# Kernel optimization log

Measured on AMD Instinct MI355X. Metric: run time of the kernel, lower is better.

Reference implementation:

```python
import jax, jax.numpy as jnp
import numpy as np
import math

D = 1024
H = 16
HD = D // H


def setup_inputs() -> dict:
    key = jax.random.key(0)
    ks = jax.random.split(key, 12)
    B, L = 2, 2048
    s = 1.0 / math.sqrt(D)
    inp = {
        "q": jax.random.normal(ks[0], (B, L, D), jnp.float32),
        "k": jax.random.normal(ks[1], (B, L, D), jnp.float32),
        "v": jax.random.normal(ks[2], (B, L, D), jnp.float32),
        "Wq": jax.random.normal(ks[3], (D, D), jnp.float32) * s,
        "bq": jnp.zeros((D,), jnp.float32),
        "Wk": jax.random.normal(ks[4], (D, D), jnp.float32) * s,
        "bk": jnp.zeros((D,), jnp.float32),
        "Wv": jax.random.normal(ks[5], (D, D), jnp.float32) * s,
        "bv": jnp.zeros((D,), jnp.float32),
        "Wo": jax.random.normal(ks[6], (D, D), jnp.float32) * s,
        "bo": jnp.zeros((D,), jnp.float32),
        "P": jax.random.normal(ks[7], (H, H), jnp.float32),  # logit_proj_pre
    }
    return inp


def _split_heads(x, B, L):
    # [B,L,D] -> [B,H,L,HD]
    return x.reshape(B, L, H, HD).transpose(0, 2, 1, 3)


def reference(q, k, v, Wq, bq, Wk, bk, Wv, bv, Wo, bo, P):
    B, L, _ = q.shape
    qh = _split_heads(q @ Wq.T + bq, B, L)
    kh = _split_heads(k @ Wk.T + bk, B, L)
    vh = _split_heads(v @ Wv.T + bv, B, L)
    # raw per-head logits [B,H,L,L]
    logits = jnp.einsum("bhld,bhmd->bhlm", qh, kh) / math.sqrt(HD)
    # talking-heads mixing across heads (pre-softmax)
    logits = jnp.einsum("bhlm,hg->bglm", logits, P)
    attn = jax.nn.softmax(logits, axis=-1)
    out = jnp.einsum("bhlm,bhmd->bhld", attn, vh)  # [B,H,L,HD]
    out = out.transpose(0, 2, 1, 3).reshape(B, L, D)
    return out @ Wo.T + bo
```

## Files before the change

kernel.cpp:

```cpp
#include <hip/hip_runtime.h>

#define D_  1024
#define H_  16
#define HD_ 64
#define L_  2048
#define B_  2
#define M_  (B_*L_)

typedef float f32x4  __attribute__((ext_vector_type(4)));
typedef short bf16x4 __attribute__((ext_vector_type(4)));
typedef short bf16x8 __attribute__((ext_vector_type(8)));

#define SRAW_PITCH 20
#define SRAW_SLAB  (16 * SRAW_PITCH)
#define VS_PITCH   24

__device__ __forceinline__ float bf2f(short s) {
    return __uint_as_float(((unsigned int)(unsigned short)s) << 16);
}
__device__ __forceinline__ short f2bf(float f) {
    unsigned u = __float_as_uint(f);
    unsigned r = (u + 0x7FFFu + ((u >> 16) & 1u)) >> 16;
    return (short)r;
}
__device__ __forceinline__ void block_sync() {
    asm volatile("s_waitcnt lgkmcnt(0)" ::: "memory");
    __builtin_amdgcn_sched_barrier(0);
    __builtin_amdgcn_s_barrier();
    __builtin_amdgcn_sched_barrier(0);
}

__global__ __launch_bounds__(256) void proj_mfma(
    const float* __restrict__ q, const float* __restrict__ k, const float* __restrict__ v,
    const float* __restrict__ Wq, const float* __restrict__ bq,
    const float* __restrict__ Wk, const float* __restrict__ bk,
    const float* __restrict__ Wv, const float* __restrict__ bv,
    short* __restrict__ qh, short* __restrict__ qlo,
    short* __restrict__ kh, short* __restrict__ vht)
{
    const int z = blockIdx.z;
    const float* X    = (z == 0) ? q  : (z == 1) ? k  : v;
    const float* W    = (z == 0) ? Wq : (z == 1) ? Wk : Wv;
    const float* bias = (z == 0) ? bq : (z == 1) ? bk : bv;

    __shared__ short Ws[128][72];
    __shared__ short Xs[128][72];

    const int tid  = threadIdx.x;
    const int w    = tid >> 6, lane = tid & 63;
    const int l16  = lane & 15, qq = lane >> 4;
    const int m0   = blockIdx.x * 128;
    const int n0   = blockIdx.y * 128;
    const int ar0  = 64 * (w & 1);
    const int br0  = 64 * (w >> 1);

    f32x4 acc[4][4] = {};

    for (int k0 = 0; k0 < D_; k0 += 64) {
        #pragma unroll
        for (int i = 0; i < 8; ++i) {
            int fidx = i * 256 + tid;
            int r = fidx >> 4, c = fidx & 15;
            float4 wv4 = *(const float4*)(W + (size_t)(n0 + r) * D_ + k0 + c * 4);
            float4 xv4 = *(const float4*)(X + (size_t)(m0 + r) * D_ + k0 + c * 4);
            bf16x4 wb = { f2bf(wv4.x), f2bf(wv4.y), f2bf(wv4.z), f2bf(wv4.w) };
            bf16x4 xb = { f2bf(xv4.x), f2bf(xv4.y), f2bf(xv4.z), f2bf(xv4.w) };
            *(bf16x4*)&Ws[r][c * 4] = wb;
            *(bf16x4*)&Xs[r][c * 4] = xb;
        }
        __syncthreads();
        bf16x8 af[2][4], bfv[2][4];
        #pragma unroll
        for (int kc = 0; kc < 2; ++kc)
            #pragma unroll
            for (int i = 0; i < 4; ++i) {
                const short* Ab = (z < 2) ? &Ws[ar0 + 16 * i + l16][kc * 32 + qq * 8]
                                          : &Xs[ar0 + 16 * i + l16][kc * 32 + qq * 8];
                const short* Bb = (z < 2) ? &Xs[br0 + 16 * i + l16][kc * 32 + qq * 8]
                                          : &Ws[br0 + 16 * i + l16][kc * 32 + qq * 8];
                af[kc][i]  = *(const bf16x8*)Ab;
                bfv[kc][i] = *(const bf16x8*)Bb;
            }
        #pragma unroll
        for (int kc = 0; kc < 2; ++kc)
            #pragma unroll
            for (int i = 0; i < 4; ++i)
                #pragma unroll
                for (int j = 0; j < 4; ++j)
                    acc[i][j] = __builtin_amdgcn_mfma_f32_16x16x32_bf16(af[kc][i], bfv[kc][j], acc[i][j], 0, 0, 0);
        __syncthreads();
    }

    if (z < 2) {
        #pragma unroll
        for (int i = 0; i < 4; ++i) {
            int nb = n0 + ar0 + 16 * i + qq * 4;
            float4 b4 = *(const float4*)(bias + nb);
            int h = nb >> 6, hd = nb & 63;
            #pragma unroll
            for (int j = 0; j < 4; ++j) {
                int m = m0 + br0 + 16 * j + l16;
                int bb = m >> 11, l = m & (L_ - 1);
                size_t o = ((((size_t)bb * H_ + h) * L_) + l) * HD_ + hd;
                f32x4 c = acc[i][j];
                float v0 = c[0] + b4.x, v1 = c[1] + b4.y, v2 = c[2] + b4.z, v3 = c[3] + b4.w;
                bf16x4 hi = { f2bf(v0), f2bf(v1), f2bf(v2), f2bf(v3) };
                if (z == 0) {
                    *(bf16x4*)&qh[o] = hi;
                    bf16x4 lo = { f2bf(v0 - bf2f(hi[0])), f2bf(v1 - bf2f(hi[1])),
                                  f2bf(v2 - bf2f(hi[2])), f2bf(v3 - bf2f(hi[3])) };
                    *(bf16x4*)&qlo[o] = lo;
                } else {
                    *(bf16x4*)&kh[o] = hi;
                }
            }
        }
    } else {
        #pragma unroll
        for (int i = 0; i < 4; ++i) {
            int mb = m0 + ar0 + 16 * i + qq * 4;
            int bb = mb >> 11, lb = mb & (L_ - 1);
            #pragma unroll
            for (int j = 0; j < 4; ++j) {
                int n = n0 + br0 + 16 * j + l16;
                int h = n >> 6, hd = n & 63;
                float bn = bias[n];
                size_t o = (((size_t)bb * H_ + h) * HD_ + hd) * (size_t)L_ + lb;
                f32x4 c = acc[i][j];
                bf16x4 ov = { f2bf(c[0] + bn), f2bf(c[1] + bn), f2bf(c[2] + bn), f2bf(c[3] + bn) };
                *(bf16x4*)&vht[o] = ov;
            }
        }
    }
}

__global__ __launch_bounds__(512, 2) void attn_mfma(
    const short* __restrict__ qh, const short* __restrict__ qlo,
    const short* __restrict__ kh, const short* __restrict__ vht,
    const float* __restrict__ P, short* __restrict__ attn_out,
    float* __restrict__ pacc, float* __restrict__ pms, int ntiles)
{
    __shared__ __align__(16) float Sraw[16 * SRAW_SLAB];
    __shared__ __align__(16) char  UPool[8 * 2 * 64 * VS_PITCH * 2];
    __shared__ float PmS[256];

    float* Smix  = (float*)UPool;
    const int tid  = threadIdx.x;
    const int n    = blockIdx.x;
    const int half = n >> 8;
    const int inr  = n & 255;
    const int b    = (inr >> 2) & 1;
    const int l0   = ((inr >> 3) * 4 + (inr & 3)) * 16;
    const int tb   = half * ntiles;
    const int w    = tid >> 6, lane = tid & 63;
    const int l16  = lane & 15, qq = lane >> 4;
    const size_t hb = (size_t)b * H_;
    short* VslabW = (short*)UPool + w * (2 * 64 * VS_PITCH);

    bf16x8 qf[2][2][2];
    #pragma unroll
    for (int hh = 0; hh < 2; ++hh)
        #pragma unroll
        for (int kc = 0; kc < 2; ++kc) {
            size_t off = ((hb + 2 * w + hh) * L_ + l0 + l16) * HD_ + kc * 32 + qq * 8;
            qf[hh][kc][0] = *(const bf16x8*)(qh  + off);
            qf[hh][kc][1] = *(const bf16x8*)(qlo + off);
        }

    int vgi_[4], vd_[4];
    const int vc = lane & 1;
    #pragma unroll
    for (int i = 0; i < 4; ++i) {
        int vrow = i * 32 + (lane >> 1);
        vgi_[i] = vrow >> 6;
        vd_[i]  = vrow & 63;
    }
    int vwoff[4];
    #pragma unroll
    for (int i = 0; i < 4; ++i)
        vwoff[i] = vgi_[i] * (64 * VS_PITCH) + vd_[i] * VS_PITCH + vc * 8;

    auto kload = [&](int tile, bf16x8 (&kdst)[2][2]) {
        const int mn = (tile & 127) * 16;
        #pragma unroll
        for (int hh = 0; hh < 2; ++hh)
            #pragma unroll
            for (int kc = 0; kc < 2; ++kc)
                kdst[hh][kc] = *(const bf16x8*)(kh + ((hb + 2 * w + hh) * L_ + mn + l16) * HD_ + kc * 32 + qq * 8);
    };
    auto vload = [&](int tile, bf16x8 (&vdst)[4]) {
        const int mn = (tile & 127) * 16;
        #pragma unroll
        for (int i = 0; i < 4; ++i)
            vdst[i] = *(const bf16x8*)(vht + ((hb + 2 * w + vgi_[i]) * HD_ + vd_[i]) * (size_t)L_ + mn + vc * 8);
    };

    bf16x8 kP[2][2], vst[4];
    kload(tb, kP); vload(tb, vst);

    if (tid < 256) PmS[tid] = P[tid] * 0.125f;

    f32x4 acc[2][4];
    #pragma unroll
    for (int dt = 0; dt < 4; ++dt) { acc[0][dt] = (f32x4){0.f,0.f,0.f,0.f}; acc[1][dt] = (f32x4){0.f,0.f,0.f,0.f}; }
    float mrun0 = 0.f, mrun1 = 0.f, srun0 = 0.f, srun1 = 0.f;

    auto qkt = [&](bf16x8 (&kr)[2][2], float* sb) {
        #pragma unroll
        for (int hh = 0; hh < 2; ++hh) {
            f32x4 s = (f32x4){0.f,0.f,0.f,0.f};
            s = __builtin_amdgcn_mfma_f32_16x16x32_bf16(kr[hh][0], qf[hh][0][0], s, 0, 0, 0);
            s = __builtin_amdgcn_mfma_f32_16x16x32_bf16(kr[hh][0], qf[hh][0][1], s, 0, 0, 0);
            s = __builtin_amdgcn_mfma_f32_16x16x32_bf16(kr[hh][1], qf[hh][1][0], s, 0, 0, 0);
            s = __builtin_amdgcn_mfma_f32_16x16x32_bf16(kr[hh][1], qf[hh][1][1], s, 0, 0, 0);
            *(f32x4*)(sb + ((2 * w + hh) * 16 + l16) * SRAW_PITCH + qq * 4) = s;
        }
    };

    qkt(kP, Sraw);
    block_sync();
    kload(tb + 1, kP);

    bf16x4 PAhi, PAlo;
    {
        float p0 = PmS[(qq * 4 + 0) * 16 + l16];
        float p1 = PmS[(qq * 4 + 1) * 16 + l16];
        float p2 = PmS[(qq * 4 + 2) * 16 + l16];
        float p3 = PmS[(qq * 4 + 3) * 16 + l16];
        PAhi = (bf16x4){ f2bf(p0), f2bf(p1), f2bf(p2), f2bf(p3) };
        PAlo = (bf16x4){ f2bf(p0 - bf2f(PAhi[0])), f2bf(p1 - bf2f(PAhi[1])),
                         f2bf(p2 - bf2f(PAhi[2])), f2bf(p3 - bf2f(PAhi[3])) };
    }

    for (int t = 0; t < ntiles; ++t) {
        {
            float2 g0 = *(const float2*)&Sraw[((qq * 4 + 0) * 16 + l16) * SRAW_PITCH + 2 * w];
            float2 g1 = *(const float2*)&Sraw[((qq * 4 + 1) * 16 + l16) * SRAW_PITCH + 2 * w];
            float2 g2 = *(const float2*)&Sraw[((qq * 4 + 2) * 16 + l16) * SRAW_PITCH + 2 * w];
            float2 g3 = *(const float2*)&Sraw[((qq * 4 + 3) * 16 + l16) * SRAW_PITCH + 2 * w];
            #pragma unroll
            for (int mi = 0; mi < 2; ++mi) {
                const int m = 2 * w + mi;
                float sv0 = mi ? g0.y : g0.x;
                float sv1 = mi ? g1.y : g1.x;
                float sv2 = mi ? g2.y : g2.x;
                float sv3 = mi ? g3.y : g3.x;
                bf16x4 bhi = { f2bf(sv0), f2bf(sv1), f2bf(sv2), f2bf(sv3) };
                bf16x4 blo = { f2bf(sv0 - bf2f(bhi[0])), f2bf(sv1 - bf2f(bhi[1])),
                               f2bf(sv2 - bf2f(bhi[2])), f2bf(sv3 - bf2f(bhi[3])) };
                f32x4 c = (f32x4){0.f, 0.f, 0.f, 0.f};
                c = __builtin_amdgcn_mfma_f32_16x16x16bf16_1k(PAhi, bhi, c, 0, 0, 0);
                c = __builtin_amdgcn_mfma_f32_16x16x16bf16_1k(PAhi, blo, c, 0, 0, 0);
                c = __builtin_amdgcn_mfma_f32_16x16x16bf16_1k(PAlo, bhi, c, 0, 0, 0);
                *(f32x4*)(Smix + (m * 16 + l16) * SRAW_PITCH + qq * 4) = c;
            }
        }
        block_sync();
        qkt(kP, Sraw);
        kload(tb + t + 2, kP);
        float sx0[4], sx1[4];
        #pragma unroll
        for (int j = 0; j < 4; ++j) {
            float2 gg = *(const float2*)&Smix[((qq * 4 + j) * 16 + l16) * SRAW_PITCH + 2 * w];
            sx0[j] = gg.x;
            sx1[j] = gg.y;
        }
        float e00 = __expf(sx0[0] - mrun0), e01 = __expf(sx0[1] - mrun0);
        float e02 = __expf(sx0[2] - mrun0), e03 = __expf(sx0[3] - mrun0);
        float e10 = __expf(sx1[0] - mrun1), e11 = __expf(sx1[1] - mrun1);
        float e12 = __expf(sx1[2] - mrun1), e13 = __expf(sx1[3] - mrun1);
        bf16x4 pf0 = { f2bf(e00), f2bf(e01), f2bf(e02), f2bf(e03) };
        bf16x4 pf1 = { f2bf(e10), f2bf(e11), f2bf(e12), f2bf(e13) };
        float t0r = fmaxf(fmaxf(sx0[0], sx0[1]), fmaxf(sx0[2], sx0[3]));
        float t1r = fmaxf(fmaxf(sx1[0], sx1[1]), fmaxf(sx1[2], sx1[3]));
        t0r = fmaxf(t0r, __shfl_xor(t0r, 16)); t0r = fmaxf(t0r, __shfl_xor(t0r, 32));
        t1r = fmaxf(t1r, __shfl_xor(t1r, 16)); t1r = fmaxf(t1r, __shfl_xor(t1r, 32));
        float ps0 = e00 + e01 + e02 + e03, ps1 = e10 + e11 + e12 + e13;
        ps0 += __shfl_xor(ps0, 16); ps0 += __shfl_xor(ps0, 32);
        ps1 += __shfl_xor(ps1, 16); ps1 += __shfl_xor(ps1, 32);
        block_sync();
        #pragma unroll
        for (int i = 0; i < 4; ++i)
            *(bf16x8*)&VslabW[vwoff[i]] = vst[i];
        #pragma unroll
        for (int i = 0; i < 2; ++i) {
            bf16x4 pf = i ? pf1 : pf0;
            #pragma unroll
            for (int dt = 0; dt < 4; ++dt) {
                bf16x4 afr = *(const bf16x4*)&VslabW[i * (64 * VS_PITCH) + (dt * 16 + l16) * VS_PITCH + qq * 4];
                acc[i][dt] = __builtin_amdgcn_mfma_f32_16x16x16bf16_1k(afr, pf, acc[i][dt], 0, 0, 0);
            }
        }
        vload(tb + t + 1, vst);
        float mnew0 = fmaxf(mrun0, t0r), mnew1 = fmaxf(mrun1, t1r);
        float corr0 = __expf(mrun0 - mnew0), corr1 = __expf(mrun1 - mnew1);
        srun0 = (srun0 + ps0) * corr0; srun1 = (srun1 + ps1) * corr1;
        acc[0][0] *= corr0; acc[0][1] *= corr0; acc[0][2] *= corr0; acc[0][3] *= corr0;
        acc[1][0] *= corr1; acc[1][1] *= corr1; acc[1][2] *= corr1; acc[1][3] *= corr1;
        mrun0 = mnew0; mrun1 = mnew1;
        block_sync();
    }

    if (pacc) {
        #pragma unroll
        for (int i = 0; i < 2; ++i) {
            int g = 2 * w + i;
            #pragma unroll
            for (int dt = 0; dt < 4; ++dt)
                *(f32x4*)&pacc[(((size_t)n * 16 + g) * 16 + l16) * 64 + dt * 16 + qq * 4] = acc[i][dt];
        }
        if (qq == 0) {
            *(float2*)&pms[(((size_t)n * 16 + 2 * w)     * 16 + l16) * 2] = make_float2(mrun0, srun0);
            *(float2*)&pms[(((size_t)n * 16 + 2 * w + 1) * 16 + l16) * 2] = make_float2(mrun1, srun1);
        }
    } else {
        float inv0 = 1.f / srun0, inv1 = 1.f / srun1;
        #pragma unroll
        for (int i = 0; i < 2; ++i) {
            float inv = i ? inv1 : inv0;
            #pragma unroll
            for (int dt = 0; dt < 4; ++dt) {
                f32x4 a = acc[i][dt];
                bf16x4 ov = { f2bf(a[0] * inv), f2bf(a[1] * inv), f2bf(a[2] * inv), f2bf(a[3] * inv) };
                *(bf16x4*)(attn_out + ((size_t)(b * L_ + l0 + l16)) * D_ + (2 * w + i) * 64 + dt * 16 + qq * 4) = ov;
            }
        }
    }
}

__global__ __launch_bounds__(256) void merge_attn(
    const float* __restrict__ pacc, const float* __restrict__ pms,
    short* __restrict__ attn)
{
    const int cid = blockIdx.x * 256 + threadIdx.x;
    const int d4 = cid & 15;
    const int g  = (cid >> 4) & 15;
    const int l  = (cid >> 8) & (L_ - 1);
    const int b  = cid >> 19;
    const int lt = l >> 4, l16 = l & 15;
    const int n0 = ((lt >> 2) << 3) + (b << 2) + (lt & 3);
    const int n1 = n0 + 256;

    float2 ms0 = *(const float2*)&pms[(((size_t)n0 * 16 + g) * 16 + l16) * 2];
    float2 ms1 = *(const float2*)&pms[(((size_t)n1 * 16 + g) * 16 + l16) * 2];
    f32x4 o0 = *(const f32x4*)&pacc[(((size_t)n0 * 16 + g) * 16 + l16) * 64 + d4 * 4];
    f32x4 o1 = *(const f32x4*)&pacc[(((size_t)n1 * 16 + g) * 16 + l16) * 64 + d4 * 4];
    float Mx = fmaxf(ms0.x, ms1.x);
    float w0 = __expf(ms0.x - Mx), w1 = __expf(ms1.x - Mx);
    float s = ms0.y * w0 + ms1.y * w1;
    float inv = 1.f / s;
    f32x4 o = o0 * w0 + o1 * w1;
    bf16x4 ov = { f2bf(o[0] * inv), f2bf(o[1] * inv), f2bf(o[2] * inv), f2bf(o[3] * inv) };
    *(bf16x4*)(attn + ((size_t)(b * L_ + l) * D_) + g * 64 + d4 * 4) = ov;
}

__global__ __launch_bounds__(256) void out_mfma(
    const short* __restrict__ attn, const float* __restrict__ Wo,
    const float* __restrict__ bo, float* __restrict__ out)
{
    __shared__ short Ws[128][72];
    __shared__ short Xs[128][72];

    const int tid = threadIdx.x;
    const int w = tid >> 6, lane = tid & 63;
    const int l16 = lane & 15, qq = lane >> 4;
    const int m0 = blockIdx.x * 128;
    const int n0 = blockIdx.y * 128;
    const int ar0 = 64 * (w & 1);
    const int br0 = 64 * (w >> 1);

    f32x4 acc[4][4] = {};

    for (int k0 = 0; k0 < D_; k0 += 64) {
        #pragma unroll
        for (int i = 0; i < 8; ++i) {
            int fidx = i * 256 + tid;
            int r = fidx >> 4, c = fidx & 15;
            float4 wv4 = *(const float4*)(Wo + (size_t)(n0 + r) * D_ + k0 + c * 4);
            bf16x4 wb = { f2bf(wv4.x), f2bf(wv4.y), f2bf(wv4.z), f2bf(wv4.w) };
            *(bf16x4*)&Ws[r][c * 4] = wb;
        }
        #pragma unroll
        for (int i = 0; i < 4; ++i) {
            int cidx = i * 256 + tid;
            int r = cidx >> 3, c = cidx & 7;
            bf16x8 xv = *(const bf16x8*)(attn + (size_t)(m0 + r) * D_ + k0 + c * 8);
            *(bf16x8*)&Xs[r][c * 8] = xv;
        }
        __syncthreads();
        bf16x8 af[2][4], bfv[2][4];
        #pragma unroll
        for (int kc = 0; kc < 2; ++kc)
            #pragma unroll
            for (int i = 0; i < 4; ++i) {
                af[kc][i]  = *(const bf16x8*)&Ws[ar0 + 16 * i + l16][kc * 32 + qq * 8];
                bfv[kc][i] = *(const bf16x8*)&Xs[br0 + 16 * i + l16][kc * 32 + qq * 8];
            }
        #pragma unroll
        for (int kc = 0; kc < 2; ++kc)
            #pragma unroll
            for (int i = 0; i < 4; ++i)
                #pragma unroll
                for (int j = 0; j < 4; ++j)
                    acc[i][j] = __builtin_amdgcn_mfma_f32_16x16x32_bf16(af[kc][i], bfv[kc][j], acc[i][j], 0, 0, 0);
        __syncthreads();
    }

    #pragma unroll
    for (int i = 0; i < 4; ++i) {
        int nb = n0 + ar0 + 16 * i + qq * 4;
        float4 b4 = *(const float4*)(bo + nb);
        #pragma unroll
        for (int j = 0; j < 4; ++j) {
            int m = m0 + br0 + 16 * j + l16;
            f32x4 c = acc[i][j];
            float4 ov = make_float4(c[0] + b4.x, c[1] + b4.y, c[2] + b4.z, c[3] + b4.w);
            *(float4*)&out[(size_t)m * D_ + nb] = ov;
        }
    }
}

extern "C" void kernel_launch(void* const* d_in, const int* in_sizes, int n_in,
                              void* d_out, int out_size, void* d_ws, size_t ws_size,
                              hipStream_t stream) {
    const float* q  = (const float*)d_in[0];
    const float* k  = (const float*)d_in[1];
    const float* v  = (const float*)d_in[2];
    const float* Wq = (const float*)d_in[3];
    const float* bq = (const float*)d_in[4];
    const float* Wk = (const float*)d_in[5];
    const float* bk = (const float*)d_in[6];
    const float* Wv = (const float*)d_in[7];
    const float* bv = (const float*)d_in[8];
    const float* Wo = (const float*)d_in[9];
    const float* bo = (const float*)d_in[10];
    const float* P  = (const float*)d_in[11];
    float* out = (float*)d_out;

    char* ws = (char*)d_ws;
    short* qh   = (short*)(ws);
    short* qlo  = (short*)(ws + (size_t)8 * 1024 * 1024);
    short* kh   = (short*)(ws + (size_t)16 * 1024 * 1024);
    short* vht  = (short*)(ws + (size_t)24 * 1024 * 1024);
    short* attn = (short*)(ws + (size_t)32 * 1024 * 1024);
    float* pacc = (float*)(ws + (size_t)40 * 1024 * 1024);
    float* pms  = (float*)(ws + (size_t)40 * 1024 * 1024 + (size_t)512 * 16 * 16 * 64 * 4);
    const size_t need2 = (size_t)40 * 1024 * 1024
                       + (size_t)512 * 16 * 16 * 64 * 4
                       + (size_t)512 * 16 * 16 * 2 * 4;
    const bool split2 = (ws_size >= need2);

    proj_mfma<<<dim3(M_ / 128, D_ / 128, 3), 256, 0, stream>>>(
        q, k, v, Wq, bq, Wk, bk, Wv, bv, qh, qlo, kh, vht);
    if (split2) {
        attn_mfma<<<dim3(512), 512, 0, stream>>>(qh, qlo, kh, vht, P, attn, pacc, pms, 64);
        merge_attn<<<dim3(4096), 256, 0, stream>>>(pacc, pms, attn);
    } else {
        attn_mfma<<<dim3(256), 512, 0, stream>>>(qh, qlo, kh, vht, P, attn, nullptr, nullptr, 128);
    }
    out_mfma<<<dim3(M_ / 128, D_ / 128), 256, 0, stream>>>(attn, Wo, bo, out);
}
```

Baseline: 359.7 us.

## Process two key tiles per attention loop iteration with double LDS buffers

The attention main loop now handles two 16-key tiles per iteration, with separate raw-score and mixed-score buffers, two sets of prefetched K/V registers, and one combined online-softmax update. This halves the block-wide barriers and softmax rescaling steps per key tile. In exchange, shared memory and register usage grow, which may reduce how many blocks fit per CU.

```diff
diff --git a/kernel.cpp b/kernel.cpp
--- a/kernel.cpp
+++ b/kernel.cpp
@@ -138,20 +138,22 @@
     const short* __restrict__ qh, const short* __restrict__ qlo,
     const short* __restrict__ kh, const short* __restrict__ vht,
     const float* __restrict__ P, short* __restrict__ attn_out,
-    float* __restrict__ pacc, float* __restrict__ pms, int ntiles)
+    float* __restrict__ pacc, float* __restrict__ pms, int nbod)
 {
-    __shared__ __align__(16) float Sraw[16 * SRAW_SLAB];
+    __shared__ __align__(16) float SrawA[16 * SRAW_SLAB];
+    __shared__ __align__(16) float SrawB[16 * SRAW_SLAB];
     __shared__ __align__(16) char  UPool[8 * 2 * 64 * VS_PITCH * 2];
     __shared__ float PmS[256];
 
-    float* Smix  = (float*)UPool;
+    float* SmixA = (float*)UPool;
+    float* SmixB = (float*)UPool + 16 * SRAW_SLAB;
     const int tid  = threadIdx.x;
     const int n    = blockIdx.x;
     const int half = n >> 8;
     const int inr  = n & 255;
     const int b    = (inr >> 2) & 1;
     const int l0   = ((inr >> 3) * 4 + (inr & 3)) * 16;
-    const int tb   = half * ntiles;
+    const int tb   = half * 64;
     const int w    = tid >> 6, lane = tid & 63;
     const int l16  = lane & 15, qq = lane >> 4;
     const size_t hb = (size_t)b * H_;
@@ -195,8 +197,9 @@
             vdst[i] = *(const bf16x8*)(vht + ((hb + 2 * w + vgi_[i]) * HD_ + vd_[i]) * (size_t)L_ + mn + vc * 8);
     };
 
-    bf16x8 kP[2][2], vst[4];
-    kload(tb, kP); vload(tb, vst);
+    bf16x8 kPa[2][2], kPb[2][2], vsta[4], vstb[4];
+    kload(tb, kPa); kload(tb + 1, kPb);
+    vload(tb, vsta); vload(tb + 1, vstb);
 
     if (tid < 256) PmS[tid] = P[tid] * 0.125f;
 
@@ -217,9 +220,10 @@
         }
     };
 
-    qkt(kP, Sraw);
+    qkt(kPa, SrawA);
+    qkt(kPb, SrawB);
     block_sync();
-    kload(tb + 1, kP);
+    kload(tb + 2, kPa); kload(tb + 3, kPb);
 
     bf16x4 PAhi, PAlo;
     {
@@ -232,66 +236,87 @@
                          f2bf(p2 - bf2f(PAhi[2])), f2bf(p3 - bf2f(PAhi[3])) };
     }
 
-    for (int t = 0; t < ntiles; ++t) {
-        {
-            float2 g0 = *(const float2*)&Sraw[((qq * 4 + 0) * 16 + l16) * SRAW_PITCH + 2 * w];
-            float2 g1 = *(const float2*)&Sraw[((qq * 4 + 1) * 16 + l16) * SRAW_PITCH + 2 * w];
-            float2 g2 = *(const float2*)&Sraw[((qq * 4 + 2) * 16 + l16) * SRAW_PITCH + 2 * w];
-            float2 g3 = *(const float2*)&Sraw[((qq * 4 + 3) * 16 + l16) * SRAW_PITCH + 2 * w];
-            #pragma unroll
-            for (int mi = 0; mi < 2; ++mi) {
-                const int m = 2 * w + mi;
-                float sv0 = mi ? g0.y : g0.x;
-                float sv1 = mi ? g1.y : g1.x;
-                float sv2 = mi ? g2.y : g2.x;
-                float sv3 = mi ? g3.y : g3.x;
-                bf16x4 bhi = { f2bf(sv0), f2bf(sv1), f2bf(sv2), f2bf(sv3) };
-                bf16x4 blo = { f2bf(sv0 - bf2f(bhi[0])), f2bf(sv1 - bf2f(bhi[1])),
-                               f2bf(sv2 - bf2f(bhi[2])), f2bf(sv3 - bf2f(bhi[3])) };
-                f32x4 c = (f32x4){0.f, 0.f, 0.f, 0.f};
-                c = __builtin_amdgcn_mfma_f32_16x16x16bf16_1k(PAhi, bhi, c, 0, 0, 0);
-                c = __builtin_amdgcn_mfma_f32_16x16x16bf16_1k(PAhi, blo, c, 0, 0, 0);
-                c = __builtin_amdgcn_mfma_f32_16x16x16bf16_1k(PAlo, bhi, c, 0, 0, 0);
-                *(f32x4*)(Smix + (m * 16 + l16) * SRAW_PITCH + qq * 4) = c;
-            }
-        }
+    auto mixpair = [&](const float* sb, float* sm) {
+        float2 g0 = *(const float2*)&sb[((qq * 4 + 0) * 16 + l16) * SRAW_PITCH + 2 * w];
+        float2 g1 = *(const float2*)&sb[((qq * 4 + 1) * 16 + l16) * SRAW_PITCH + 2 * w];
+        float2 g2 = *(const float2*)&sb[((qq * 4 + 2) * 16 + l16) * SRAW_PITCH + 2 * w];
+        float2 g3 = *(const float2*)&sb[((qq * 4 + 3) * 16 + l16) * SRAW_PITCH + 2 * w];
+        #pragma unroll
+        for (int mi = 0; mi < 2; ++mi) {
+            const int m = 2 * w + mi;
+            float sv0 = mi ? g0.y : g0.x;
+            float sv1 = mi ? g1.y : g1.x;
+            float sv2 = mi ? g2.y : g2.x;
+            float sv3 = mi ? g3.y : g3.x;
+            bf16x4 bhi = { f2bf(sv0), f2bf(sv1), f2bf(sv2), f2bf(sv3) };
+            bf16x4 blo = { f2bf(sv0 - bf2f(bhi[0])), f2bf(sv1 - bf2f(bhi[1])),
+                           f2bf(sv2 - bf2f(bhi[2])), f2bf(sv3 - bf2f(bhi[3])) };
+            f32x4 c = (f32x4){0.f, 0.f, 0.f, 0.f};
+            c = __builtin_amdgcn_mfma_f32_16x16x16bf16_1k(PAhi, bhi, c, 0, 0, 0);
+            c = __builtin_amdgcn_mfma_f32_16x16x16bf16_1k(PAhi, blo, c, 0, 0, 0);
+            c = __builtin_amdgcn_mfma_f32_16x16x16bf16_1k(PAlo, bhi, c, 0, 0, 0);
+            *(f32x4*)(sm + (m * 16 + l16) * SRAW_PITCH + qq * 4) = c;
+        }
+    };
+
+    auto stage_pv = [&](bf16x8 (&vst)[4], bf16x4 pf0, bf16x4 pf1) {
+        #pragma unroll
+        for (int i = 0; i < 4; ++i)
+            *(bf16x8*)&VslabW[vwoff[i]] = vst[i];
+        #pragma unroll
+        for (int i = 0; i < 2; ++i) {
+            bf16x4 pf = i ? pf1 : pf0;
+            #pragma unroll
+            for (int dt = 0; dt < 4; ++dt) {
+                bf16x4 afr = *(const bf16x4*)&VslabW[i * (64 * VS_PITCH) + (dt * 16 + l16) * VS_PITCH + qq * 4];
+                acc[i][dt] = __builtin_amdgcn_mfma_f32_16x16x16bf16_1k(afr, pf, acc[i][dt], 0, 0, 0);
+            }
+        }
+    };
+
+    for (int t = 0; t < nbod; ++t) {
+        mixpair(SrawA, SmixA);
+        mixpair(SrawB, SmixB);
         block_sync();
-        qkt(kP, Sraw);
-        kload(tb + t + 2, kP);
-        float sx0[4], sx1[4];
+        float sxA0[4], sxA1[4], sxB0[4], sxB1[4];
         #pragma unroll
         for (int j = 0; j < 4; ++j) {
-            float2 gg = *(const float2*)&Smix[((qq * 4 + j) * 16 + l16) * SRAW_PITCH + 2 * w];
-            sx0[j] = gg.x;
-            sx1[j] = gg.y;
-        }
-        float e00 = __expf(sx0[0] - mrun0), e01 = __expf(sx0[1] - mrun0);
-        float e02 = __expf(sx0[2] - mrun0), e03 = __expf(sx0[3] - mrun0);
-        float e10 = __expf(sx1[0] - mrun1), e11 = __expf(sx1[1] - mrun1);
-        float e12 = __expf(sx1[2] - mrun1), e13 = __expf(sx1[3] - mrun1);
-        bf16x4 pf0 = { f2bf(e00), f2bf(e01), f2bf(e02), f2bf(e03) };
-        bf16x4 pf1 = { f2bf(e10), f2bf(e11), f2bf(e12), f2bf(e13) };
-        float t0r = fmaxf(fmaxf(sx0[0], sx0[1]), fmaxf(sx0[2], sx0[3]));
-        float t1r = fmaxf(fmaxf(sx1[0], sx1[1]), fmaxf(sx1[2], sx1[3]));
+            float2 ga = *(const float2*)&SmixA[((qq * 4 + j) * 16 + l16) * SRAW_PITCH + 2 * w];
+            float2 gb = *(const float2*)&SmixB[((qq * 4 + j) * 16 + l16) * SRAW_PITCH + 2 * w];
+            sxA0[j] = ga.x; sxA1[j] = ga.y;
+            sxB0[j] = gb.x; sxB1[j] = gb.y;
+        }
+        float eA00 = __expf(sxA0[0] - mrun0), eA01 = __expf(sxA0[1] - mrun0);
+        float eA02 = __expf(sxA0[2] - mrun0), eA03 = __expf(sxA0[3] - mrun0);
+        float eA10 = __expf(sxA1[0] - mrun1), eA11 = __expf(sxA1[1] - mrun1);
+        float eA12 = __expf(sxA1[2] - mrun1), eA13 = __expf(sxA1[3] - mrun1);
+        float eB00 = __expf(sxB0[0] - mrun0), eB01 = __expf(sxB0[1] - mrun0);
+        float eB02 = __expf(sxB0[2] - mrun0), eB03 = __expf(sxB0[3] - mrun0);
+        float eB10 = __expf(sxB1[0] - mrun1), eB11 = __expf(sxB1[1] - mrun1);
+        float eB12 = __expf(sxB1[2] - mrun1), eB13 = __expf(sxB1[3] - mrun1);
+        bf16x4 pfA0 = { f2bf(eA00), f2bf(eA01), f2bf(eA02), f2bf(eA03) };
+        bf16x4 pfA1 = { f2bf(eA10), f2bf(eA11), f2bf(eA12), f2bf(eA13) };
+        bf16x4 pfB0 = { f2bf(eB00), f2bf(eB01), f2bf(eB02), f2bf(eB03) };
+        bf16x4 pfB1 = { f2bf(eB10), f2bf(eB11), f2bf(eB12), f2bf(eB13) };
+        float t0r = fmaxf(fmaxf(fmaxf(sxA0[0], sxA0[1]), fmaxf(sxA0[2], sxA0[3])),
+                          fmaxf(fmaxf(sxB0[0], sxB0[1]), fmaxf(sxB0[2], sxB0[3])));
+        float t1r = fmaxf(fmaxf(fmaxf(sxA1[0], sxA1[1]), fmaxf(sxA1[2], sxA1[3])),
+                          fmaxf(fmaxf(sxB1[0], sxB1[1]), fmaxf(sxB1[2], sxB1[3])));
         t0r = fmaxf(t0r, __shfl_xor(t0r, 16)); t0r = fmaxf(t0r, __shfl_xor(t0r, 32));
         t1r = fmaxf(t1r, __shfl_xor(t1r, 16)); t1r = fmaxf(t1r, __shfl_xor(t1r, 32));
-        float ps0 = e00 + e01 + e02 + e03, ps1 = e10 + e11 + e12 + e13;
+        float ps0 = (eA00 + eA01 + eA02 + eA03) + (eB00 + eB01 + eB02 + eB03);
+        float ps1 = (eA10 + eA11 + eA12 + eA13) + (eB10 + eB11 + eB12 + eB13);
         ps0 += __shfl_xor(ps0, 16); ps0 += __shfl_xor(ps0, 32);
         ps1 += __shfl_xor(ps1, 16); ps1 += __shfl_xor(ps1, 32);
         block_sync();
-        #pragma unroll
-        for (int i = 0; i < 4; ++i)
-            *(bf16x8*)&VslabW[vwoff[i]] = vst[i];
-        #pragma unroll
-        for (int i = 0; i < 2; ++i) {
-            bf16x4 pf = i ? pf1 : pf0;
-            #pragma unroll
-            for (int dt = 0; dt < 4; ++dt) {
-                bf16x4 afr = *(const bf16x4*)&VslabW[i * (64 * VS_PITCH) + (dt * 16 + l16) * VS_PITCH + qq * 4];
-                acc[i][dt] = __builtin_amdgcn_mfma_f32_16x16x16bf16_1k(afr, pf, acc[i][dt], 0, 0, 0);
-            }
-        }
-        vload(tb + t + 1, vst);
+        stage_pv(vsta, pfA0, pfA1);
+        vload(tb + 2 * t + 2, vsta);
+        stage_pv(vstb, pfB0, pfB1);
+        vload(tb + 2 * t + 3, vstb);
+        qkt(kPa, SrawA);
+        qkt(kPb, SrawB);
+        kload(tb + 2 * t + 4, kPa);
+        kload(tb + 2 * t + 5, kPb);
         float mnew0 = fmaxf(mrun0, t0r), mnew1 = fmaxf(mrun1, t1r);
         float corr0 = __expf(mrun0 - mnew0), corr1 = __expf(mrun1 - mnew1);
         srun0 = (srun0 + ps0) * corr0; srun1 = (srun1 + ps1) * corr1;
@@ -453,10 +478,10 @@
     proj_mfma<<<dim3(M_ / 128, D_ / 128, 3), 256, 0, stream>>>(
         q, k, v, Wq, bq, Wk, bk, Wv, bv, qh, qlo, kh, vht);
     if (split2) {
-        attn_mfma<<<dim3(512), 512, 0, stream>>>(qh, qlo, kh, vht, P, attn, pacc, pms, 64);
+        attn_mfma<<<dim3(512), 512, 0, stream>>>(qh, qlo, kh, vht, P, attn, pacc, pms, 32);
         merge_attn<<<dim3(4096), 256, 0, stream>>>(pacc, pms, attn);
     } else {
-        attn_mfma<<<dim3(256), 512, 0, stream>>>(qh, qlo, kh, vht, P, attn, nullptr, nullptr, 128);
+        attn_mfma<<<dim3(256), 512, 0, stream>>>(qh, qlo, kh, vht, P, attn, nullptr, nullptr, 64);
     }
     out_mfma<<<dim3(M_ / 128, D_ / 128), 256, 0, stream>>>(attn, Wo, bo, out);
 }
```

After: 411.1 us. +14.3%, slower.
